# Performance work log

Hardware: AMD Instinct MI355X
Metric: run time of the kernel (lower is better)

## Reference

```python
import jax, jax.numpy as jnp
import numpy as np

N_NODES = 20000
N_EDGES = 160000
N_GRAPHS = 64
DIMS = [9, 128, 256, 512, 1534]
NEG_SLOPE_ATT = 0.2   # GATConv attention LeakyReLU
NEG_SLOPE_ACT = 0.01  # nn.LeakyReLU between layers
EPS = 1e-5            # GraphNorm eps


def setup_inputs() -> dict:
    key = jax.random.key(0)
    inp = {}
    k, key = jax.random.split(key)
    inp['x'] = jax.random.normal(k, (N_NODES, DIMS[0]), jnp.float32)
    k, key = jax.random.split(key)
    inp['edge_index'] = jax.random.randint(k, (2, N_EDGES), 0, N_NODES)
    k, key = jax.random.split(key)
    inp['batch'] = jnp.sort(jax.random.randint(k, (N_NODES,), 0, N_GRAPHS))
    for l in range(4):
        din, dout = DIMS[l], DIMS[l + 1]
        k1, k2, k3, key = jax.random.split(key, 4)
        s = 1.0 / np.sqrt(din)
        inp[f'W{l}'] = (jax.random.normal(k1, (din, dout)) * s).astype(jnp.float32)
        inp[f'asrc{l}'] = (jax.random.normal(k2, (dout,)) * 0.1).astype(jnp.float32)
        inp[f'adst{l}'] = (jax.random.normal(k3, (dout,)) * 0.1).astype(jnp.float32)
        inp[f'b{l}'] = jnp.zeros((dout,), jnp.float32)
        inp[f'g{l}'] = jnp.ones((dout,), jnp.float32)   # GraphNorm weight
        inp[f'bt{l}'] = jnp.zeros((dout,), jnp.float32)  # GraphNorm bias
        inp[f'ms{l}'] = jnp.ones((dout,), jnp.float32)   # GraphNorm mean_scale
    return inp


def _gat_conv(h, src, dst, n, W, asrc, adst, b):
    # PyG GATConv, heads=1: linear (no bias), edge attention, segment softmax, scatter-add
    hp = h @ W                                                    # [N, dout]
    e = jax.nn.leaky_relu((hp @ asrc)[src] + (hp @ adst)[dst], NEG_SLOPE_ATT)  # [E]
    m = jax.ops.segment_max(e, dst, num_segments=n)
    m = jnp.where(jnp.isfinite(m), m, 0.0)
    ex = jnp.exp(e - m[dst])
    denom = jax.ops.segment_sum(ex, dst, num_segments=n)
    alpha = ex / (denom[dst] + 1e-16)                             # [E]
    out = jax.ops.segment_sum(alpha[:, None] * hp[src], dst, num_segments=n)
    return out + b


def _graph_norm(h, batch, counts, g, bt, ms):
    # PyG GraphNorm: per-graph mean/var with learnable mean_scale
    mean = jax.ops.segment_sum(h, batch, num_segments=N_GRAPHS) / counts
    out = h - ms * mean[batch]
    var = jax.ops.segment_sum(out * out, batch, num_segments=N_GRAPHS) / counts
    return out / jnp.sqrt(var[batch] + EPS) * g + bt


def _forward(x, edge_index, batch, params):
    n = x.shape[0]
    loops = jnp.arange(n)
    src = jnp.concatenate([edge_index[0], loops])   # GATConv add_self_loops=True
    dst = jnp.concatenate([edge_index[1], loops])
    counts = jax.ops.segment_sum(jnp.ones((n,), x.dtype), batch, num_segments=N_GRAPHS)[:, None]
    h = x
    for (W, asrc, adst, b, g, bt, ms) in params:
        h = _gat_conv(h, src, dst, n, W, asrc, adst, b)
        h = jax.nn.leaky_relu(h, NEG_SLOPE_ACT)
        h = _graph_norm(h, batch, counts, g, bt, ms)
        # Dropout(p=0.1) is identity in eval mode
    mean = (jax.ops.segment_sum(h, batch, num_segments=N_GRAPHS) / counts)[:, None, :]
    mx = jax.ops.segment_max(h, batch, num_segments=N_GRAPHS)[:, None, :]
    return jnp.concatenate([mean, mx], axis=1)      # [G, 2, 1534]


def reference(x, edge_index, batch,
              W0, asrc0, adst0, b0, g0, bt0, ms0,
              W1, asrc1, adst1, b1, g1, bt1, ms1,
              W2, asrc2, adst2, b2, g2, bt2, ms2,
              W3, asrc3, adst3, b3, g3, bt3, ms3):
    params = [
        (W0, asrc0, adst0, b0, g0, bt0, ms0),
        (W1, asrc1, adst1, b1, g1, bt1, ms1),
        (W2, asrc2, adst2, b2, g2, bt2, ms2),
        (W3, asrc3, adst3, b3, g3, bt3, ms3),
    ]
    return _forward(x, edge_index, batch, params)
```

## Files before the change

### kernel.cpp

```cpp
#include <hip/hip_runtime.h>
#include <math.h>

typedef unsigned int u32;
typedef unsigned short u16;
using half8 = __attribute__((ext_vector_type(8))) _Float16;
using f32x4 = __attribute__((ext_vector_type(4))) float;

#define NN 20000
#define MPAD 20096
#define NE 160000
#define ET 180000
#define NG 64
#define NBLK 79

constexpr float NEG_ATT = 0.2f;
constexpr float NEG_ACT = 0.01f;
constexpr float EPS_GN  = 1e-5f;

struct Ptr4 { const float *p0, *p1, *p2, *p3; };


__device__ __forceinline__ u16 f2h(float f) {
    _Float16 h = (_Float16)f;
    return __builtin_bit_cast(u16, h);
}
__device__ __forceinline__ float h2f(u16 b) {
    return (float)__builtin_bit_cast(_Float16, b);
}

__device__ __forceinline__ void gl_lds16(const void* g, void* l) {
    __builtin_amdgcn_global_load_lds((const __attribute__((address_space(1))) u32*)g,
                                     (__attribute__((address_space(3))) u32*)l, 16, 0, 0);
}

__device__ __forceinline__ float lrelu_att(float v) {
    return (v > 0.f) ? v : NEG_ATT * v;
}


__global__ void k_bounds(const int* __restrict__ batch, int* __restrict__ counts,
                         int* __restrict__ gstart) {
    __shared__ int ls[NG + 1];
    int g = threadIdx.x;
    int lo = 0, hi = NN;
    while (lo < hi) {
        int mid = (lo + hi) >> 1;
        if (batch[mid] < g) lo = mid + 1; else hi = mid;
    }
    ls[g] = lo;
    if (g == 0) ls[NG] = NN;
    __syncthreads();
    counts[g] = ls[g + 1] - ls[g];
    gstart[g] = ls[g];
    if (g == 0) gstart[NG] = NN;
}


__global__ void k_deg(const int* __restrict__ ei, int* deg) {
    int i = blockIdx.x * 256 + threadIdx.x;
    if (i >= ET) return;
    int dst = (i < NE) ? ei[NE + i] : (i - NE);
    atomicAdd(&deg[dst], 1);
}

__global__ void k_scan1(const int* __restrict__ deg, int* __restrict__ bsum) {
    int i = blockIdx.x * 256 + threadIdx.x;
    int v = (i < NN) ? deg[i] : 0;
    int lane = threadIdx.x & 63, w = threadIdx.x >> 6;
    #pragma unroll
    for (int off = 32; off; off >>= 1) v += __shfl_down(v, off, 64);
    __shared__ int ws[4];
    if (lane == 0) ws[w] = v;
    __syncthreads();
    if (threadIdx.x == 0) bsum[blockIdx.x] = ws[0] + ws[1] + ws[2] + ws[3];
}

__global__ void k_scan2(const int* __restrict__ bsum, int* __restrict__ boff,
                        int* __restrict__ total) {
    int tid = threadIdx.x;
    int v = (tid < NBLK) ? bsum[tid] : 0;
    int lane = tid & 63, w = tid >> 6;
    int val = v;
    #pragma unroll
    for (int off = 1; off < 64; off <<= 1) {
        int t = __shfl_up(val, off, 64);
        if (lane >= off) val += t;
    }
    __shared__ int ws[4];
    if (lane == 63) ws[w] = val;
    __syncthreads();
    int woff = 0;
    for (int k = 0; k < w; k++) woff += ws[k];
    int excl = woff + val - v;
    if (tid < NBLK) boff[tid] = excl;
    if (tid == NBLK - 1) *total = excl + v;
}

__global__ void k_scan3(const int* __restrict__ deg, const int* __restrict__ boff,
                        int* __restrict__ row_ptr, int* __restrict__ cursor) {
    int i = blockIdx.x * 256 + threadIdx.x;
    int v = (i < NN) ? deg[i] : 0;
    int lane = threadIdx.x & 63, w = threadIdx.x >> 6;
    int val = v;
    #pragma unroll
    for (int off = 1; off < 64; off <<= 1) {
        int t = __shfl_up(val, off, 64);
        if (lane >= off) val += t;
    }
    __shared__ int ws[4];
    if (lane == 63) ws[w] = val;
    __syncthreads();
    int woff = 0;
    for (int k = 0; k < w; k++) woff += ws[k];
    int excl = boff[blockIdx.x] + woff + val - v;
    if (i < NN) { row_ptr[i] = excl; cursor[i] = excl; }
}

__global__ void k_scatter(const int* __restrict__ ei, int* cursor, int* __restrict__ col) {
    int i = blockIdx.x * 256 + threadIdx.x;
    if (i >= ET) return;
    int s, d;
    if (i < NE) { s = ei[i]; d = ei[NE + i]; } else { s = i - NE; d = s; }
    int p = atomicAdd(&cursor[d], 1);
    col[p] = s;
}


__global__ void k_wvec_all(Ptr4 W, Ptr4 As, Ptr4 Ad,
                           float* __restrict__ wsrcA, float* __restrict__ wdstA) {
    const int dins[4]  = {9, 128, 256, 512};
    const int douts[4] = {128, 256, 512, 1534};
    int l = blockIdx.y, k = blockIdx.x;
    if (k >= dins[l]) return;
    const float* Wp = (l == 0) ? W.p0 : (l == 1) ? W.p1 : (l == 2) ? W.p2 : W.p3;
    const float* as = (l == 0) ? As.p0 : (l == 1) ? As.p1 : (l == 2) ? As.p2 : As.p3;
    const float* ad = (l == 0) ? Ad.p0 : (l == 1) ? Ad.p1 : (l == 2) ? Ad.p2 : Ad.p3;
    int NC = douts[l];
    const float* row = Wp + (size_t)k * NC;
    float ss = 0.f, sd = 0.f;
    for (int n = threadIdx.x; n < NC; n += 256) {
        float w = row[n];
        ss += w * as[n];
        sd += w * ad[n];
    }
    __shared__ float ls[8];
    int lane = threadIdx.x & 63, w4 = threadIdx.x >> 6;
    #pragma unroll
    for (int off = 32; off; off >>= 1) {
        ss += __shfl_down(ss, off, 64);
        sd += __shfl_down(sd, off, 64);
    }
    if (lane == 0) { ls[w4] = ss; ls[4 + w4] = sd; }
    __syncthreads();
    if (threadIdx.x == 0) {
        wsrcA[l * 512 + k] = ls[0] + ls[1] + ls[2] + ls[3];
        wdstA[l * 512 + k] = ls[4] + ls[5] + ls[6] + ls[7];
    }
}


__global__ void k_wbt_all(Ptr4 W, u16* __restrict__ WbTall) {
    const int Ks[3] = {128, 256, 512};
    const int NCs[3] = {256, 512, 1534};
    const int Nps[3] = {256, 512, 1536};
    const size_t offs[3] = {0, 256 * 128, 256 * 128 + 512 * 256};
    int l = blockIdx.z;
    int K = Ks[l], NC = NCs[l], Np = Nps[l];
    int n0 = blockIdx.x * 32, k0 = blockIdx.y * 32;
    if (n0 >= Np || k0 >= K) return;
    const float* Wp = (l == 0) ? W.p1 : (l == 1) ? W.p2 : W.p3;
    u16* WbT = WbTall + offs[l];
    __shared__ u16 tile[32][33];
    int tx = threadIdx.x & 31, ty = threadIdx.x >> 5;
    #pragma unroll
    for (int i = 0; i < 4; i++) {
        int k = k0 + ty + i * 8, n = n0 + tx;
        float v = (k < K && n < NC) ? Wp[(size_t)k * NC + n] : 0.f;
        tile[ty + i * 8][tx] = f2h(v);
    }
    __syncthreads();
    #pragma unroll
    for (int i = 0; i < 4; i++) {
        int n = n0 + ty + i * 8, k = k0 + tx;
        if (n < Np && k < K) WbT[(size_t)n * K + k] = tile[tx][ty + i * 8];
    }
}


__global__ void k_scores0(const float* __restrict__ x, const float* __restrict__ wsrc,
                          const float* __restrict__ wdst, float* __restrict__ s_src,
                          float* __restrict__ s_dst) {
    int v = blockIdx.x * 256 + threadIdx.x;
    if (v >= NN) return;
    const float* r = x + (size_t)v * 9;
    float ss = 0.f, sd = 0.f;
    #pragma unroll
    for (int k = 0; k < 9; k++) { ss += r[k] * wsrc[k]; sd += r[k] * wdst[k]; }
    s_src[v] = ss; s_dst[v] = sd;
}

template <int VW>
__global__ void k_scores_h(const u16* __restrict__ h, const float* __restrict__ wsrc,
                           const float* __restrict__ wdst, float* __restrict__ s_src,
                           float* __restrict__ s_dst, int din) {
    int v = blockIdx.x * 4 + (threadIdx.x >> 6);
    int lane = threadIdx.x & 63;
    if (v >= NN) return;
    const u16* row = h + (size_t)v * din;
    float ss = 0.f, sd = 0.f;
    for (int d = lane * VW; d < din; d += 64 * VW) {
        u32 ua[VW / 2];
        if constexpr (VW == 2) {
            ua[0] = *(const u32*)(row + d);
        } else if constexpr (VW == 4) {
            uint2 t = *(const uint2*)(row + d);
            ua[0] = t.x; ua[1] = t.y;
        } else {
            uint4 t = *(const uint4*)(row + d);
            ua[0] = t.x; ua[1] = t.y; ua[2] = t.z; ua[3] = t.w;
        }
        #pragma unroll
        for (int j = 0; j < VW / 2; j++) {
            float h0 = h2f((u16)(ua[j] & 0xffffu)), h1 = h2f((u16)(ua[j] >> 16));
            ss += h0 * wsrc[d + 2 * j] + h1 * wsrc[d + 2 * j + 1];
            sd += h0 * wdst[d + 2 * j] + h1 * wdst[d + 2 * j + 1];
        }
    }
    #pragma unroll
    for (int off = 32; off; off >>= 1) {
        ss += __shfl_down(ss, off, 64);
        sd += __shfl_down(sd, off, 64);
    }
    if (lane == 0) { s_src[v] = ss; s_dst[v] = sd; }
}


__global__ __launch_bounds__(256) void k_alpha(const int* __restrict__ row_ptr,
                                               const int* __restrict__ col,
                                               const float* __restrict__ s_src,
                                               const float* __restrict__ s_dst,
                                               float* __restrict__ alpha) {
    int grp = threadIdx.x >> 6;
    int lane = threadIdx.x & 63;
    int v = blockIdx.x * 4 + grp;
    if (v >= NN) return;
    int st = row_ptr[v], en = row_ptr[v + 1];
    float sd = s_dst[v];
    float mx = -INFINITY;
    for (int p = st + lane; p < en; p += 64)
        mx = fmaxf(mx, lrelu_att(s_src[col[p]] + sd));
    #pragma unroll
    for (int off = 32; off; off >>= 1) mx = fmaxf(mx, __shfl_xor(mx, off, 64));
    float sum = 0.f;
    for (int p = st + lane; p < en; p += 64)
        sum += __expf(lrelu_att(s_src[col[p]] + sd) - mx);
    #pragma unroll
    for (int off = 32; off; off >>= 1) sum += __shfl_xor(sum, off, 64);
    float inv = 1.0f / (sum + 1e-16f);
    for (int p = st + lane; p < en; p += 64)
        alpha[p] = __expf(lrelu_att(s_src[col[p]] + sd) - mx) * inv;
}


template <int TPN, int CPT>
__global__ __launch_bounds__(256) void k_agg2(const u16* __restrict__ h,
                                              const int* __restrict__ row_ptr,
                                              const int* __restrict__ col,
                                              const float* __restrict__ alpha,
                                              u16* __restrict__ agg, int din) {
    constexpr int NPB = 256 / TPN;
    int grp = threadIdx.x / TPN;
    int lane = threadIdx.x % TPN;
    int v = blockIdx.x * NPB + grp;
    if (v >= NN) return;
    int st = row_ptr[v], en = row_ptr[v + 1];
    int d0 = lane * 2 * CPT;
    const u16* hb = h + d0;
    float acc[2 * CPT];
    #pragma unroll
    for (int i = 0; i < 2 * CPT; i++) acc[i] = 0.f;

    auto fma1 = [&](int c, float a) {
        if constexpr (CPT == 1) {
            u32 t = *(const u32*)(hb + (size_t)c * din);
            acc[0] += a * h2f((u16)(t & 0xffffu));
            acc[1] += a * h2f((u16)(t >> 16));
        } else {
            uint2 t = *(const uint2*)(hb + (size_t)c * din);
            acc[0] += a * h2f((u16)(t.x & 0xffffu));
            acc[1] += a * h2f((u16)(t.x >> 16));
            acc[2] += a * h2f((u16)(t.y & 0xffffu));
            acc[3] += a * h2f((u16)(t.y >> 16));
        }
    };

    int p = st;
    for (; p + 4 <= en; p += 4) {
        int c0 = col[p], c1 = col[p + 1], c2 = col[p + 2], c3 = col[p + 3];
        float a0 = alpha[p], a1 = alpha[p + 1], a2 = alpha[p + 2], a3 = alpha[p + 3];
        if constexpr (CPT == 1) {
            u32 t0 = *(const u32*)(hb + (size_t)c0 * din);
            u32 t1 = *(const u32*)(hb + (size_t)c1 * din);
            u32 t2 = *(const u32*)(hb + (size_t)c2 * din);
            u32 t3 = *(const u32*)(hb + (size_t)c3 * din);
            acc[0] += a0 * h2f((u16)(t0 & 0xffffu)) + a1 * h2f((u16)(t1 & 0xffffu))
                    + a2 * h2f((u16)(t2 & 0xffffu)) + a3 * h2f((u16)(t3 & 0xffffu));
            acc[1] += a0 * h2f((u16)(t0 >> 16)) + a1 * h2f((u16)(t1 >> 16))
                    + a2 * h2f((u16)(t2 >> 16)) + a3 * h2f((u16)(t3 >> 16));
        } else {
            uint2 t0 = *(const uint2*)(hb + (size_t)c0 * din);
            uint2 t1 = *(const uint2*)(hb + (size_t)c1 * din);
            uint2 t2 = *(const uint2*)(hb + (size_t)c2 * din);
            uint2 t3 = *(const uint2*)(hb + (size_t)c3 * din);
            acc[0] += a0 * h2f((u16)(t0.x & 0xffffu)) + a1 * h2f((u16)(t1.x & 0xffffu))
                    + a2 * h2f((u16)(t2.x & 0xffffu)) + a3 * h2f((u16)(t3.x & 0xffffu));
            acc[1] += a0 * h2f((u16)(t0.x >> 16)) + a1 * h2f((u16)(t1.x >> 16))
                    + a2 * h2f((u16)(t2.x >> 16)) + a3 * h2f((u16)(t3.x >> 16));
            acc[2] += a0 * h2f((u16)(t0.y & 0xffffu)) + a1 * h2f((u16)(t1.y & 0xffffu))
                    + a2 * h2f((u16)(t2.y & 0xffffu)) + a3 * h2f((u16)(t3.y & 0xffffu));
            acc[3] += a0 * h2f((u16)(t0.y >> 16)) + a1 * h2f((u16)(t1.y >> 16))
                    + a2 * h2f((u16)(t2.y >> 16)) + a3 * h2f((u16)(t3.y >> 16));
        }
    }
    for (; p < en; p++) fma1(col[p], alpha[p]);

    if constexpr (CPT == 1) {
        u32 o = (u32)f2h(acc[0]) | ((u32)f2h(acc[1]) << 16);
        *(u32*)(agg + (size_t)v * din + d0) = o;
    } else {
        uint2 ov;
        ov.x = (u32)f2h(acc[0]) | ((u32)f2h(acc[1]) << 16);
        ov.y = (u32)f2h(acc[2]) | ((u32)f2h(acc[3]) << 16);
        *(uint2*)(agg + (size_t)v * din + d0) = ov;
    }
}

__global__ __launch_bounds__(256) void k_agg0_fused(const float* __restrict__ x,
                                                    const int* __restrict__ row_ptr,
                                                    const int* __restrict__ col,
                                                    const float* __restrict__ s_src,
                                                    const float* __restrict__ s_dst,
                                                    float* __restrict__ agg0) {
    __shared__ float sm[4 * 2];
    int grp = threadIdx.x >> 6;
    int lane = threadIdx.x & 63;
    int v = blockIdx.x * 4 + grp;
    bool valid = v < NN;
    int st = 0, en = 0;
    float sd = 0.f;
    if (valid) { st = row_ptr[v]; en = row_ptr[v + 1]; sd = s_dst[v]; }
    float mx = -INFINITY;
    if (valid) {
        for (int p = st + lane; p < en; p += 64)
            mx = fmaxf(mx, lrelu_att(s_src[col[p]] + sd));
    }
    #pragma unroll
    for (int off = 32; off; off >>= 1) mx = fmaxf(mx, __shfl_xor(mx, off, 64));
    float sum = 0.f;
    if (valid) {
        for (int p = st + lane; p < en; p += 64)
            sum += __expf(lrelu_att(s_src[col[p]] + sd) - mx);
    }
    #pragma unroll
    for (int off = 32; off; off >>= 1) sum += __shfl_xor(sum, off, 64);
    if (lane == 0) { sm[grp * 2] = mx; sm[grp * 2 + 1] = 1.0f / (sum + 1e-16f); }
    __syncthreads();
    if (!valid || lane >= 9) return;
    float m = sm[grp * 2], inv = sm[grp * 2 + 1];
    float acc = 0.f;
    for (int p = st; p < en; p++) {
        int c = col[p];
        float a = __expf(lrelu_att(s_src[c] + sd) - m);
        acc += a * x[(size_t)c * 9 + lane];
    }
    agg0[(size_t)v * 9 + lane] = acc * inv;
}


__global__ __launch_bounds__(256) void k_gemm0(const float* __restrict__ agg0,
                                               const float* __restrict__ W,
                                               const float* __restrict__ bias,
                                               u16* __restrict__ out) {
    __shared__ float Ws[9 * 128];
    for (int i = threadIdx.x; i < 9 * 128; i += 256) Ws[i] = W[i];
    __syncthreads();
    int node = blockIdx.x * 2 + (threadIdx.x >> 7);
    int n = threadIdx.x & 127;
    if (node >= NN) return;
    const float* xr = agg0 + (size_t)node * 9;
    float acc = bias[n];
    #pragma unroll
    for (int k = 0; k < 9; k++) acc += xr[k] * Ws[k * 128 + n];
    acc = (acc > 0.f) ? acc : NEG_ACT * acc;
    out[(size_t)node * 128 + n] = f2h(acc);
}


#define BM 128
#define BK 32

__global__ __launch_bounds__(256) void k_gemm_f16(const u16* __restrict__ A,
                                                  const u16* __restrict__ B,
                                                  const float* __restrict__ bias,
                                                  u16* __restrict__ C,
                                                  int K, int ldC, int NC, int ntx) {
    int nwg = gridDim.x;
    int b = blockIdx.x;
    int q = nwg >> 3, r = nwg & 7;
    int xcd = b & 7, idx = b >> 3;
    int wg = (xcd < r ? xcd * (q + 1) : r * (q + 1) + (xcd - r) * q) + idx;
    int row0 = (wg / ntx) * BM;
    int col0 = (wg % ntx) * BM;

    __shared__ u16 lds[2][2][BM * BK];
    int tid = threadIdx.x;
    int lane = tid & 63, w = tid >> 6;
    int wr = w >> 1, wc = w & 1;

    f32x4 acc[4][4];
    #pragma unroll
    for (int m = 0; m < 4; m++)
        #pragma unroll
        for (int n = 0; n < 4; n++)
            #pragma unroll
            for (int rr2 = 0; rr2 < 4; rr2++) acc[m][n][rr2] = 0.f;

    int nt = K / BK;

    auto stage = [&](int buf, int t) {
        int k0 = t * BK;
        #pragma unroll
        for (int c = 0; c < 2; c++) {
            int idx2 = tid + c * 256;
            int rr2 = idx2 >> 2, kc = idx2 & 3;
            int kcs = kc ^ (rr2 & 3);
            gl_lds16(A + (size_t)(row0 + rr2) * K + k0 + kcs * 8, &lds[buf][0][idx2 * 8]);
            gl_lds16(B + (size_t)(col0 + rr2) * K + k0 + kcs * 8, &lds[buf][1][idx2 * 8]);
        }
    };

    auto compute = [&](int buf) {
        const u16* As = &lds[buf][0][0];
        const u16* Bs = &lds[buf][1][0];
        int kg = lane >> 4, rl = lane & 15;
        half8 af[4], bfr[4];
        #pragma unroll
        for (int m = 0; m < 4; m++) {
            int rr2 = wr * 64 + m * 16 + rl;
            af[m] = *(const half8*)(As + rr2 * BK + (kg ^ (rr2 & 3)) * 8);
        }
        #pragma unroll
        for (int n = 0; n < 4; n++) {
            int rr2 = wc * 64 + n * 16 + rl;
            bfr[n] = *(const half8*)(Bs + rr2 * BK + (kg ^ (rr2 & 3)) * 8);
        }
        #pragma unroll
        for (int m = 0; m < 4; m++)
            #pragma unroll
            for (int n = 0; n < 4; n++)
                acc[m][n] = __builtin_amdgcn_mfma_f32_16x16x32_f16(af[m], bfr[n], acc[m][n], 0, 0, 0);
    };

    stage(0, 0);
    __syncthreads();
    for (int t = 0; t < nt; t++) {
        if (t + 1 < nt) stage((t + 1) & 1, t + 1);
        compute(t & 1);
        __syncthreads();
    }

    u16* ep = ((u16*)lds) + w * (32 * 72);
    int kg = lane >> 4, rl = lane & 15;
    int rrow = lane >> 3;
    int c8 = (lane & 7) * 8;
    #pragma unroll
    for (int half = 0; half < 2; half++) {
        #pragma unroll
        for (int m2 = 0; m2 < 2; m2++) {
            int m = half * 2 + m2;
            #pragma unroll
            for (int n = 0; n < 4; n++) {
                int colg = col0 + wc * 64 + n * 16 + rl;
                float bb = (colg < NC) ? bias[colg] : 0.f;
                #pragma unroll
                for (int rr2 = 0; rr2 < 4; rr2++) {
                    float o = acc[m][n][rr2] + bb;
                    o = (o > 0.f) ? o : NEG_ACT * o;
                    ep[(m2 * 16 + kg * 4 + rr2) * 72 + n * 16 + rl] = f2h(o);
                }
            }
        }
        #pragma unroll
        for (int it = 0; it < 4; it++) {
            int rloc = it * 8 + rrow;
            half8 vv = *(const half8*)(ep + rloc * 72 + c8);
            int rowg = row0 + wr * 64 + half * 32 + rloc;
            *(half8*)(C + (size_t)rowg * ldC + col0 + wc * 64 + c8) = vv;
        }
    }
}


__global__ __launch_bounds__(1024, 4) void k_gemm256(const u16* __restrict__ A,
                                                     const u16* __restrict__ B,
                                                     const float* __restrict__ bias,
                                                     u16* __restrict__ C,
                                                     int K, int ldC, int NC, int ntx, int M) {
    __shared__ u16 sMem[49152];

    int nwg = gridDim.x, b = blockIdx.x;
    int q = nwg >> 3, r = nwg & 7;
    int xcd = b & 7, bidx = b >> 3;
    int wg = (xcd < r ? xcd * (q + 1) : r * (q + 1) + (xcd - r) * q) + bidx;
    int row0 = (wg / ntx) * 256;
    int col0 = (wg % ntx) * 256;

    int tid = threadIdx.x;
    int w = tid >> 6, lane = tid & 63;
    int wm = w >> 2, wn = w & 3;
    int rl = lane & 15, kg = lane >> 4;
    int ksl = (kg ^ ((rl >> 1) & 3)) * 8;

    f32x4 acc[4][4];
    #pragma unroll
    for (int m = 0; m < 4; m++)
        #pragma unroll
        for (int n = 0; n < 4; n++)
            #pragma unroll
            for (int i = 0; i < 4; i++) acc[m][n][i] = 0.f;

    {
        int rr = tid >> 2, s = tid & 3;
        int ss = s ^ ((rr >> 1) & 3);
        int ra = row0 + rr; ra = (ra < M) ? ra : (M - 1);
        const u16* aSrc0 = A + (size_t)ra * K + ss * 8;
        const u16* bSrc0 = B + (size_t)(col0 + rr) * K + ss * 8;
        u16* dstA = sMem + tid * 8;
        u16* dstB = sMem + 8192 + tid * 8;

        auto stage = [&](int t, int bf2) {
            gl_lds16(aSrc0 + t * 32, dstA + bf2 * 16384);
            gl_lds16(bSrc0 + t * 32, dstB + bf2 * 16384);
        };

        half8 af[4], bf[4];
        auto ldAB = [&](int bf2) {
            const u16* Ab = sMem + bf2 * 16384;
            const u16* Bb = Ab + 8192;
            #pragma unroll
            for (int i = 0; i < 4; i++)
                af[i] = *(const half8*)(Ab + (wm * 64 + i * 16 + rl) * 32 + ksl);
            #pragma unroll
            for (int i = 0; i < 4; i++)
                bf[i] = *(const half8*)(Bb + (wn * 64 + i * 16 + rl) * 32 + ksl);
        };

        int nt = K >> 5;

        stage(0, 0); stage(1, 1);
        __builtin_amdgcn_sched_barrier(0);
        asm volatile("s_waitcnt vmcnt(2)" ::: "memory");
        __builtin_amdgcn_s_barrier();
        __builtin_amdgcn_sched_barrier(0);

        int rb = 0;
        for (int t = 0; t < nt; t++) {
            int sb = rb + 2; if (sb >= 3) sb -= 3;
            if (t + 2 < nt) stage(t + 2, sb);
            ldAB(rb);
            __builtin_amdgcn_s_setprio(1);
            #pragma unroll
            for (int i = 0; i < 4; i++)
                #pragma unroll
                for (int n = 0; n < 4; n++)
                    acc[i][n] = __builtin_amdgcn_mfma_f32_16x16x32_f16(af[i], bf[n], acc[i][n], 0, 0, 0);
            __builtin_amdgcn_s_setprio(0);
            __builtin_amdgcn_sched_barrier(0);
            if (t + 2 < nt)      asm volatile("s_waitcnt vmcnt(2)" ::: "memory");
            else if (t + 1 < nt) asm volatile("s_waitcnt vmcnt(0)" ::: "memory");
            __builtin_amdgcn_s_barrier();
            __builtin_amdgcn_sched_barrier(0);
            rb = (rb == 2) ? 0 : rb + 1;
        }
    }

    u16* ep = sMem + w * (32 * 72);
    float bv[4];
    #pragma unroll
    for (int n = 0; n < 4; n++) {
        int colg = col0 + wn * 64 + n * 16 + rl;
        bv[n] = (colg < NC) ? bias[colg] : 0.f;
    }
    int rrow = lane >> 3, c8 = (lane & 7) * 8;
    #pragma unroll
    for (int mh = 0; mh < 2; mh++) {
        #pragma unroll
        for (int msub = 0; msub < 2; msub++) {
            int m = mh * 2 + msub;
            #pragma unroll
            for (int n = 0; n < 4; n++) {
                #pragma unroll
                for (int rg = 0; rg < 4; rg++) {
                    float o = acc[m][n][rg] + bv[n];
                    o = (o > 0.f) ? o : NEG_ACT * o;
                    ep[(msub * 16 + kg * 4 + rg) * 72 + n * 16 + rl] = f2h(o);
                }
            }
        }
        #pragma unroll
        for (int it = 0; it < 4; it++) {
            int rloc = it * 8 + rrow;
            half8 vv = *(const half8*)(ep + rloc * 72 + c8);
            int rowg = row0 + wm * 64 + mh * 32 + rloc;
            if (rowg < M)
                *(half8*)(C + (size_t)rowg * ldC + col0 + wn * 64 + c8) = vv;
        }
    }
}


__global__ __launch_bounds__(256) void k_gn_fused(const u16* __restrict__ h,
                           const int* __restrict__ gstart,
                           const float* __restrict__ ms, const float* __restrict__ gam,
                           const float* __restrict__ bet, u16* __restrict__ out, int ld) {
    int g = blockIdx.x;
    int c0 = blockIdx.y * 128;
    int ct = threadIdx.x & 15, rg = threadIdx.x >> 4;
    int d0 = c0 + ct * 8;
    int st = gstart[g], en = gstart[g + 1];
    float inv = 1.0f / (float)(en - st);
    float s[8], qq[8];
    #pragma unroll
    for (int i = 0; i < 8; i++) { s[i] = 0.f; qq[i] = 0.f; }
    for (int r = st + rg; r < en; r += 16) {
        uint4 u = *(const uint4*)(h + (size_t)r * ld + d0);
        u32 ua[4] = {u.x, u.y, u.z, u.w};
        #pragma unroll
        for (int j = 0; j < 4; j++) {
            float v0 = h2f((u16)(ua[j] & 0xffffu)), v1 = h2f((u16)(ua[j] >> 16));
            s[2 * j] += v0; s[2 * j + 1] += v1;
            qq[2 * j] += v0 * v0; qq[2 * j + 1] += v1 * v1;
        }
    }
    __shared__ float Ls[16][128], Lq[16][128];
    #pragma unroll
    for (int i = 0; i < 8; i++) { Ls[rg][ct * 8 + i] = s[i]; Lq[rg][ct * 8 + i] = qq[i]; }
    __syncthreads();
    int tid = threadIdx.x;
    if (tid < 128) {
        float ss = 0.f, sq = 0.f;
        #pragma unroll
        for (int r2 = 1; r2 < 16; r2++) { ss += Ls[r2][tid]; sq += Lq[r2][tid]; }
        Ls[0][tid] += ss; Lq[0][tid] += sq;
    }
    __syncthreads();
    float sub[8], sc[8], bv[8];
    #pragma unroll
    for (int i = 0; i < 8; i++) {
        int cl = ct * 8 + i, d = d0 + i;
        float msv = ms[d];
        float mean = Ls[0][cl] * inv;
        float q2   = Lq[0][cl] * inv;
        float var  = fmaxf(q2 - (2.f * msv - msv * msv) * mean * mean, 0.f);
        sub[i] = msv * mean;
        sc[i]  = gam[d] * rsqrtf(var + EPS_GN);
        bv[i]  = bet[d];
    }
    for (int r = st + rg; r < en; r += 16) {
        uint4 u = *(const uint4*)(h + (size_t)r * ld + d0);
        u32 ua[4] = {u.x, u.y, u.z, u.w};
        uint4 wv4;
        u32 wo[4];
        #pragma unroll
        for (int j = 0; j < 4; j++) {
            float o0 = (h2f((u16)(ua[j] & 0xffffu)) - sub[2 * j]) * sc[2 * j] + bv[2 * j];
            float o1 = (h2f((u16)(ua[j] >> 16)) - sub[2 * j + 1]) * sc[2 * j + 1] + bv[2 * j + 1];
            wo[j] = (u32)f2h(o0) | ((u32)f2h(o1) << 16);
        }
        wv4.x = wo[0]; wv4.y = wo[1]; wv4.z = wo[2]; wv4.w = wo[3];
        *(uint4*)(out + (size_t)r * ld + d0) = wv4;
    }
}

__global__ __launch_bounds__(256) void k_gn_poolf(const u16* __restrict__ h,
                           const int* __restrict__ gstart,
                           const float* __restrict__ ms, const float* __restrict__ gam,
                           const float* __restrict__ bet, float* __restrict__ out,
                           int dout, int ld) {
    int g = blockIdx.x;
    int c0 = blockIdx.y * 128;
    int ct = threadIdx.x & 15, rg = threadIdx.x >> 4;
    int d0 = c0 + ct * 8;
    int st = gstart[g], en = gstart[g + 1];
    float inv = 1.0f / (float)(en - st);
    float s[8], qq[8];
    #pragma unroll
    for (int i = 0; i < 8; i++) { s[i] = 0.f; qq[i] = 0.f; }
    for (int r = st + rg; r < en; r += 16) {
        uint4 u = *(const uint4*)(h + (size_t)r * ld + d0);
        u32 ua[4] = {u.x, u.y, u.z, u.w};
        #pragma unroll
        for (int j = 0; j < 4; j++) {
            float v0 = h2f((u16)(ua[j] & 0xffffu)), v1 = h2f((u16)(ua[j] >> 16));
            s[2 * j] += v0; s[2 * j + 1] += v1;
            qq[2 * j] += v0 * v0; qq[2 * j + 1] += v1 * v1;
        }
    }
    __shared__ float Ls[16][128], Lq[16][128];
    #pragma unroll
    for (int i = 0; i < 8; i++) { Ls[rg][ct * 8 + i] = s[i]; Lq[rg][ct * 8 + i] = qq[i]; }
    __syncthreads();
    int tid = threadIdx.x;
    if (tid < 128) {
        float ss = 0.f, sq = 0.f;
        #pragma unroll
        for (int r2 = 1; r2 < 16; r2++) { ss += Ls[r2][tid]; sq += Lq[r2][tid]; }
        Ls[0][tid] += ss; Lq[0][tid] += sq;
    }
    __syncthreads();
    float sub[8], sc[8], bv[8];
    #pragma unroll
    for (int i = 0; i < 8; i++) {
        int cl = ct * 8 + i, d = d0 + i;
        int dc = (d < dout) ? d : (dout - 1);
        float msv = ms[dc];
        float mean = Ls[0][cl] * inv;
        float q2   = Lq[0][cl] * inv;
        float var  = fmaxf(q2 - (2.f * msv - msv * msv) * mean * mean, 0.f);
        sub[i] = msv * mean;
        sc[i]  = gam[dc] * rsqrtf(var + EPS_GN);
        bv[i]  = bet[dc];
    }
    float ps[8], pm[8];
    #pragma unroll
    for (int i = 0; i < 8; i++) { ps[i] = 0.f; pm[i] = -INFINITY; }
    for (int r = st + rg; r < en; r += 16) {
        uint4 u = *(const uint4*)(h + (size_t)r * ld + d0);
        u32 ua[4] = {u.x, u.y, u.z, u.w};
        #pragma unroll
        for (int j = 0; j < 4; j++) {
            float o0 = (h2f((u16)(ua[j] & 0xffffu)) - sub[2 * j]) * sc[2 * j] + bv[2 * j];
            float o1 = (h2f((u16)(ua[j] >> 16)) - sub[2 * j + 1]) * sc[2 * j + 1] + bv[2 * j + 1];
            ps[2 * j] += o0; ps[2 * j + 1] += o1;
            pm[2 * j] = fmaxf(pm[2 * j], o0); pm[2 * j + 1] = fmaxf(pm[2 * j + 1], o1);
        }
    }
    __syncthreads();
    #pragma unroll
    for (int i = 0; i < 8; i++) { Ls[rg][ct * 8 + i] = ps[i]; Lq[rg][ct * 8 + i] = pm[i]; }
    __syncthreads();
    if (tid < 128) {
        float ss = 0.f, mm = -INFINITY;
        #pragma unroll
        for (int r2 = 0; r2 < 16; r2++) { ss += Ls[r2][tid]; mm = fmaxf(mm, Lq[r2][tid]); }
        int d = c0 + tid;
        if (d < dout) {
            out[(size_t)g * 2 * dout + d] = ss * inv;
            out[(size_t)g * 2 * dout + dout + d] = mm;
        }
    }
}


extern "C" void kernel_launch(void* const* d_in, const int* in_sizes, int n_in,
                              void* d_out, int out_size, void* d_ws, size_t ws_size,
                              hipStream_t stream) {
    const float* x = (const float*)d_in[0];
    const int* ei = (const int*)d_in[1];
    const int* batch = (const int*)d_in[2];
    const float *Wl[4], *Asr[4], *Ads[4], *Bi[4], *Ga[4], *Be[4], *Ms[4];
    for (int l = 0; l < 4; l++) {
        int b = 3 + 7 * l;
        Wl[l]  = (const float*)d_in[b];
        Asr[l] = (const float*)d_in[b + 1];
        Ads[l] = (const float*)d_in[b + 2];
        Bi[l]  = (const float*)d_in[b + 3];
        Ga[l]  = (const float*)d_in[b + 4];
        Be[l]  = (const float*)d_in[b + 5];
        Ms[l]  = (const float*)d_in[b + 6];
    }

    char* ws = (char*)d_ws;
    size_t off = 0;
    auto alloc = [&](size_t bytes) -> char* {
        char* p = ws + off;
        off += (bytes + 255) & ~(size_t)255;
        return p;
    };
    u16*   actA   = (u16*)alloc((size_t)MPAD * 512 * 2);
    u16*   actB   = (u16*)alloc((size_t)MPAD * 1536 * 2);
    u16*   agg    = (u16*)alloc((size_t)MPAD * 512 * 2);
    float* agg0   = (float*)alloc((size_t)NN * 9 * 4);
    u16*   WbTall = (u16*)alloc((size_t)(256 * 128 + 512 * 256 + 1536 * 512) * 2);
    float* wsrcA  = (float*)alloc((size_t)4 * 512 * 4);
    float* wdstA  = (float*)alloc((size_t)4 * 512 * 4);
    float* s_src  = (float*)alloc((size_t)NN * 4);
    float* s_dst  = (float*)alloc((size_t)NN * 4);
    float* alpha  = (float*)alloc((size_t)ET * 4);
    int* row_ptr  = (int*)alloc((size_t)(NN + 1) * 4);
    int* cursor   = (int*)alloc((size_t)NN * 4);
    int* colA     = (int*)alloc((size_t)ET * 4);
    int* counts   = (int*)alloc((size_t)NG * 4);
    int* gstart   = (int*)alloc((size_t)(NG + 1) * 4);
    int* bsum     = (int*)alloc((size_t)NBLK * 4);
    int* boff     = (int*)alloc((size_t)NBLK * 4);

    char* zbase = ws + off;
    int* deg      = (int*)alloc((size_t)NN * 4);
    size_t zbytes = (size_t)((ws + off) - zbase);
    hipMemsetAsync(zbase, 0, zbytes, stream);

    k_bounds<<<1, 64, 0, stream>>>(batch, counts, gstart);
    k_deg<<<(ET + 255) / 256, 256, 0, stream>>>(ei, deg);
    k_scan1<<<NBLK, 256, 0, stream>>>(deg, bsum);
    k_scan2<<<1, 256, 0, stream>>>(bsum, boff, row_ptr + NN);
    k_scan3<<<NBLK, 256, 0, stream>>>(deg, boff, row_ptr, cursor);
    k_scatter<<<(ET + 255) / 256, 256, 0, stream>>>(ei, cursor, colA);

    Ptr4 Wp{Wl[0], Wl[1], Wl[2], Wl[3]};
    Ptr4 Ap{Asr[0], Asr[1], Asr[2], Asr[3]};
    Ptr4 Dp{Ads[0], Ads[1], Ads[2], Ads[3]};
    k_wvec_all<<<dim3(512, 4), 256, 0, stream>>>(Wp, Ap, Dp, wsrcA, wdstA);
    k_wbt_all<<<dim3(48, 16, 3), 256, 0, stream>>>(Wp, WbTall);

    const int dims[5] = {9, 128, 256, 512, 1534};
    const size_t wbtOffs[3] = {0, 256 * 128, 256 * 128 + 512 * 256};
    const int RT256 = (MPAD + 255) / 256;

    for (int l = 0; l < 4; l++) {
        int din = dims[l], dout = dims[l + 1];
        int ldo = (dout == 1534) ? 1536 : dout;
        const float* wsrc = wsrcA + l * 512;
        const float* wdst = wdstA + l * 512;

        if (l == 0) {
            k_scores0<<<(NN + 255) / 256, 256, 0, stream>>>(x, wsrc, wdst, s_src, s_dst);
            k_agg0_fused<<<(NN + 3) / 4, 256, 0, stream>>>(x, row_ptr, colA, s_src, s_dst, agg0);
            k_gemm0<<<(NN + 1) / 2, 256, 0, stream>>>(agg0, Wl[0], Bi[0], actB);
        } else {
            if (din == 128)
                k_scores_h<2><<<(NN + 3) / 4, 256, 0, stream>>>(actA, wsrc, wdst, s_src, s_dst, din);
            else if (din == 256)
                k_scores_h<4><<<(NN + 3) / 4, 256, 0, stream>>>(actA, wsrc, wdst, s_src, s_dst, din);
            else
                k_scores_h<8><<<(NN + 3) / 4, 256, 0, stream>>>(actA, wsrc, wdst, s_src, s_dst, din);
            k_alpha<<<(NN + 3) / 4, 256, 0, stream>>>(row_ptr, colA, s_src, s_dst, alpha);
            if (din == 128)
                k_agg2<64, 1><<<(NN + 3) / 4, 256, 0, stream>>>(actA, row_ptr, colA, alpha, agg, din);
            else if (din == 256)
                k_agg2<64, 2><<<(NN + 3) / 4, 256, 0, stream>>>(actA, row_ptr, colA, alpha, agg, din);
            else
                k_agg2<128, 2><<<(NN + 1) / 2, 256, 0, stream>>>(actA, row_ptr, colA, alpha, agg, din);
            if (l == 1) {
                int ntx = ldo / 128;
                int nwg = ntx * (MPAD / 128);
                k_gemm_f16<<<nwg, 256, 0, stream>>>(agg, WbTall + wbtOffs[0], Bi[1], actB,
                                                    din, ldo, dout, ntx);
            } else {
                int ntx = ldo / 256;
                int nwg = ntx * RT256;
                k_gemm256<<<nwg, 1024, 0, stream>>>(agg, WbTall + wbtOffs[l - 1], Bi[l], actB,
                                                    din, ldo, dout, ntx, MPAD);
            }
        }

        if (l < 3)
            k_gn_fused<<<dim3(NG, ldo / 128), 256, 0, stream>>>(actB, gstart,
                                                                Ms[l], Ga[l], Be[l], actA, ldo);
        else
            k_gn_poolf<<<dim3(NG, 12), 256, 0, stream>>>(actB, gstart,
                                                         Ms[3], Ga[3], Be[3], (float*)d_out,
                                                         1534, 1536);
    }
}
```

Before: 327.1 us.

## Single-pass final GraphNorm+pool, wider agg loads, smaller GEMM for layer 2

The final GraphNorm plus pooling kernel now reads the activations once, collecting per-column sum, sum of squares, min and max. It derives the normalized mean and max analytically, choosing the min or max depending on the sign of the affine scale, instead of making a second pass over the data. The aggregation kernel is generalized to 16-byte loads (CPT=4), so din=512 uses 64 threads per node. Layer 2 is switched from the 256-tile GEMM to the 128-tile f16 GEMM. These aim to cut memory traffic and tune the mid-size GEMM, at some risk of poorer GEMM efficiency for layer 2.

```diff
diff --git a/kernel.cpp b/kernel.cpp
--- a/kernel.cpp
+++ b/kernel.cpp
@@ -280,58 +280,59 @@
     #pragma unroll
     for (int i = 0; i < 2 * CPT; i++) acc[i] = 0.f;
 
-    auto fma1 = [&](int c, float a) {
+    auto ld = [&](int c, u32* t) {
         if constexpr (CPT == 1) {
-            u32 t = *(const u32*)(hb + (size_t)c * din);
-            acc[0] += a * h2f((u16)(t & 0xffffu));
-            acc[1] += a * h2f((u16)(t >> 16));
+            t[0] = *(const u32*)(hb + (size_t)c * din);
+        } else if constexpr (CPT == 2) {
+            uint2 u = *(const uint2*)(hb + (size_t)c * din);
+            t[0] = u.x; t[1] = u.y;
         } else {
-            uint2 t = *(const uint2*)(hb + (size_t)c * din);
-            acc[0] += a * h2f((u16)(t.x & 0xffffu));
-            acc[1] += a * h2f((u16)(t.x >> 16));
-            acc[2] += a * h2f((u16)(t.y & 0xffffu));
-            acc[3] += a * h2f((u16)(t.y >> 16));
+            uint4 u = *(const uint4*)(hb + (size_t)c * din);
+            t[0] = u.x; t[1] = u.y; t[2] = u.z; t[3] = u.w;
         }
     };
 
     int p = st;
     for (; p + 4 <= en; p += 4) {
-        int c0 = col[p], c1 = col[p + 1], c2 = col[p + 2], c3 = col[p + 3];
-        float a0 = alpha[p], a1 = alpha[p + 1], a2 = alpha[p + 2], a3 = alpha[p + 3];
-        if constexpr (CPT == 1) {
-            u32 t0 = *(const u32*)(hb + (size_t)c0 * din);
-            u32 t1 = *(const u32*)(hb + (size_t)c1 * din);
-            u32 t2 = *(const u32*)(hb + (size_t)c2 * din);
-            u32 t3 = *(const u32*)(hb + (size_t)c3 * din);
-            acc[0] += a0 * h2f((u16)(t0 & 0xffffu)) + a1 * h2f((u16)(t1 & 0xffffu))
-                    + a2 * h2f((u16)(t2 & 0xffffu)) + a3 * h2f((u16)(t3 & 0xffffu));
-            acc[1] += a0 * h2f((u16)(t0 >> 16)) + a1 * h2f((u16)(t1 >> 16))
-                    + a2 * h2f((u16)(t2 >> 16)) + a3 * h2f((u16)(t3 >> 16));
-        } else {
-            uint2 t0 = *(const uint2*)(hb + (size_t)c0 * din);
-            uint2 t1 = *(const uint2*)(hb + (size_t)c1 * din);
-            uint2 t2 = *(const uint2*)(hb + (size_t)c2 * din);
-            uint2 t3 = *(const uint2*)(hb + (size_t)c3 * din);
-            acc[0] += a0 * h2f((u16)(t0.x & 0xffffu)) + a1 * h2f((u16)(t1.x & 0xffffu))
-                    + a2 * h2f((u16)(t2.x & 0xffffu)) + a3 * h2f((u16)(t3.x & 0xffffu));
-            acc[1] += a0 * h2f((u16)(t0.x >> 16)) + a1 * h2f((u16)(t1.x >> 16))
-                    + a2 * h2f((u16)(t2.x >> 16)) + a3 * h2f((u16)(t3.x >> 16));
-            acc[2] += a0 * h2f((u16)(t0.y & 0xffffu)) + a1 * h2f((u16)(t1.y & 0xffffu))
-                    + a2 * h2f((u16)(t2.y & 0xffffu)) + a3 * h2f((u16)(t3.y & 0xffffu));
-            acc[3] += a0 * h2f((u16)(t0.y >> 16)) + a1 * h2f((u16)(t1.y >> 16))
-                    + a2 * h2f((u16)(t2.y >> 16)) + a3 * h2f((u16)(t3.y >> 16));
-        }
-    }
-    for (; p < en; p++) fma1(col[p], alpha[p]);
-
+        float aa[4];
+        u32 t[4][CPT];
+        #pragma unroll
+        for (int e = 0; e < 4; e++) {
+            int c = col[p + e];
+            aa[e] = alpha[p + e];
+            ld(c, t[e]);
+        }
+        #pragma unroll
+        for (int e = 0; e < 4; e++)
+            #pragma unroll
+            for (int j = 0; j < CPT; j++) {
+                acc[2 * j]     += aa[e] * h2f((u16)(t[e][j] & 0xffffu));
+                acc[2 * j + 1] += aa[e] * h2f((u16)(t[e][j] >> 16));
+            }
+    }
+    for (; p < en; p++) {
+        float a = alpha[p];
+        u32 t[CPT];
+        ld(col[p], t);
+        #pragma unroll
+        for (int j = 0; j < CPT; j++) {
+            acc[2 * j]     += a * h2f((u16)(t[j] & 0xffffu));
+            acc[2 * j + 1] += a * h2f((u16)(t[j] >> 16));
+        }
+    }
+
+    u32 o[CPT];
+    #pragma unroll
+    for (int j = 0; j < CPT; j++)
+        o[j] = (u32)f2h(acc[2 * j]) | ((u32)f2h(acc[2 * j + 1]) << 16);
     if constexpr (CPT == 1) {
-        u32 o = (u32)f2h(acc[0]) | ((u32)f2h(acc[1]) << 16);
-        *(u32*)(agg + (size_t)v * din + d0) = o;
+        *(u32*)(agg + (size_t)v * din + d0) = o[0];
+    } else if constexpr (CPT == 2) {
+        uint2 ov; ov.x = o[0]; ov.y = o[1];
+        *(uint2*)(agg + (size_t)v * din + d0) = ov;
     } else {
-        uint2 ov;
-        ov.x = (u32)f2h(acc[0]) | ((u32)f2h(acc[1]) << 16);
-        ov.y = (u32)f2h(acc[2]) | ((u32)f2h(acc[3]) << 16);
-        *(uint2*)(agg + (size_t)v * din + d0) = ov;
+        uint4 ov; ov.x = o[0]; ov.y = o[1]; ov.z = o[2]; ov.w = o[3];
+        *(uint4*)(agg + (size_t)v * din + d0) = ov;
     }
 }
 
@@ -682,6 +683,7 @@
     }
 }
 
+
 __global__ __launch_bounds__(256) void k_gn_poolf(const u16* __restrict__ h,
                            const int* __restrict__ gstart,
                            const float* __restrict__ ms, const float* __restrict__ gam,
@@ -693,9 +695,9 @@
     int d0 = c0 + ct * 8;
     int st = gstart[g], en = gstart[g + 1];
     float inv = 1.0f / (float)(en - st);
-    float s[8], qq[8];
-    #pragma unroll
-    for (int i = 0; i < 8; i++) { s[i] = 0.f; qq[i] = 0.f; }
+    float s[8], qq[8], mn[8], mx[8];
+    #pragma unroll
+    for (int i = 0; i < 8; i++) { s[i] = 0.f; qq[i] = 0.f; mn[i] = INFINITY; mx[i] = -INFINITY; }
     for (int r = st + rg; r < en; r += 16) {
         uint4 u = *(const uint4*)(h + (size_t)r * ld + d0);
         u32 ua[4] = {u.x, u.y, u.z, u.w};
@@ -704,59 +706,36 @@
             float v0 = h2f((u16)(ua[j] & 0xffffu)), v1 = h2f((u16)(ua[j] >> 16));
             s[2 * j] += v0; s[2 * j + 1] += v1;
             qq[2 * j] += v0 * v0; qq[2 * j + 1] += v1 * v1;
-        }
-    }
-    __shared__ float Ls[16][128], Lq[16][128];
-    #pragma unroll
-    for (int i = 0; i < 8; i++) { Ls[rg][ct * 8 + i] = s[i]; Lq[rg][ct * 8 + i] = qq[i]; }
+            mn[2 * j] = fminf(mn[2 * j], v0); mn[2 * j + 1] = fminf(mn[2 * j + 1], v1);
+            mx[2 * j] = fmaxf(mx[2 * j], v0); mx[2 * j + 1] = fmaxf(mx[2 * j + 1], v1);
+        }
+    }
+    __shared__ float Ls[16][128], Lq[16][128], Ln[16][128], Lx[16][128];
+    #pragma unroll
+    for (int i = 0; i < 8; i++) {
+        Ls[rg][ct * 8 + i] = s[i]; Lq[rg][ct * 8 + i] = qq[i];
+        Ln[rg][ct * 8 + i] = mn[i]; Lx[rg][ct * 8 + i] = mx[i];
+    }
     __syncthreads();
     int tid = threadIdx.x;
     if (tid < 128) {
-        float ss = 0.f, sq = 0.f;
-        #pragma unroll
-        for (int r2 = 1; r2 < 16; r2++) { ss += Ls[r2][tid]; sq += Lq[r2][tid]; }
-        Ls[0][tid] += ss; Lq[0][tid] += sq;
-    }
-    __syncthreads();
-    float sub[8], sc[8], bv[8];
-    #pragma unroll
-    for (int i = 0; i < 8; i++) {
-        int cl = ct * 8 + i, d = d0 + i;
-        int dc = (d < dout) ? d : (dout - 1);
-        float msv = ms[dc];
-        float mean = Ls[0][cl] * inv;
-        float q2   = Lq[0][cl] * inv;
-        float var  = fmaxf(q2 - (2.f * msv - msv * msv) * mean * mean, 0.f);
-        sub[i] = msv * mean;
-        sc[i]  = gam[dc] * rsqrtf(var + EPS_GN);
-        bv[i]  = bet[dc];
-    }
-    float ps[8], pm[8];
-    #pragma unroll
-    for (int i = 0; i < 8; i++) { ps[i] = 0.f; pm[i] = -INFINITY; }
-    for (int r = st + rg; r < en; r += 16) {
-        uint4 u = *(const uint4*)(h + (size_t)r * ld + d0);
-        u32 ua[4] = {u.x, u.y, u.z, u.w};
-        #pragma unroll
-        for (int j = 0; j < 4; j++) {
-            float o0 = (h2f((u16)(ua[j] & 0xffffu)) - sub[2 * j]) * sc[2 * j] + bv[2 * j];
-            float o1 = (h2f((u16)(ua[j] >> 16)) - sub[2 * j + 1]) * sc[2 * j + 1] + bv[2 * j + 1];
-            ps[2 * j] += o0; ps[2 * j + 1] += o1;
-            pm[2 * j] = fmaxf(pm[2 * j], o0); pm[2 * j + 1] = fmaxf(pm[2 * j + 1], o1);
-        }
-    }
-    __syncthreads();
-    #pragma unroll
-    for (int i = 0; i < 8; i++) { Ls[rg][ct * 8 + i] = ps[i]; Lq[rg][ct * 8 + i] = pm[i]; }
-    __syncthreads();
-    if (tid < 128) {
-        float ss = 0.f, mm = -INFINITY;
-        #pragma unroll
-        for (int r2 = 0; r2 < 16; r2++) { ss += Ls[r2][tid]; mm = fmaxf(mm, Lq[r2][tid]); }
+        float ss = 0.f, sq = 0.f, amn = INFINITY, amx = -INFINITY;
+        #pragma unroll
+        for (int r2 = 0; r2 < 16; r2++) {
+            ss += Ls[r2][tid]; sq += Lq[r2][tid];
+            amn = fminf(amn, Ln[r2][tid]); amx = fmaxf(amx, Lx[r2][tid]);
+        }
         int d = c0 + tid;
         if (d < dout) {
-            out[(size_t)g * 2 * dout + d] = ss * inv;
-            out[(size_t)g * 2 * dout + dout + d] = mm;
+            float msv = ms[d];
+            float mean = ss * inv;
+            float q2   = sq * inv;
+            float var  = fmaxf(q2 - (2.f * msv - msv * msv) * mean * mean, 0.f);
+            float sc   = gam[d] * rsqrtf(var + EPS_GN);
+            float off  = bet[d] - msv * mean * sc;
+            out[(size_t)g * 2 * dout + d] = (mean - msv * mean) * sc + bet[d];
+            float mval = (sc >= 0.f) ? amx : amn;
+            out[(size_t)g * 2 * dout + dout + d] = mval * sc + off;
         }
     }
 }
@@ -850,11 +829,11 @@
             else if (din == 256)
                 k_agg2<64, 2><<<(NN + 3) / 4, 256, 0, stream>>>(actA, row_ptr, colA, alpha, agg, din);
             else
-                k_agg2<128, 2><<<(NN + 1) / 2, 256, 0, stream>>>(actA, row_ptr, colA, alpha, agg, din);
-            if (l == 1) {
+                k_agg2<64, 4><<<(NN + 3) / 4, 256, 0, stream>>>(actA, row_ptr, colA, alpha, agg, din);
+            if (l <= 2) {
                 int ntx = ldo / 128;
                 int nwg = ntx * (MPAD / 128);
-                k_gemm_f16<<<nwg, 256, 0, stream>>>(agg, WbTall + wbtOffs[0], Bi[1], actB,
+                k_gemm_f16<<<nwg, 256, 0, stream>>>(agg, WbTall + wbtOffs[l - 1], Bi[l], actB,
                                                     din, ldo, dout, ntx);
             } else {
                 int ntx = ldo / 256;
```

Result: faster. 308.3 us (-5.7%).
